# Performance work log

Measured on AMD Instinct MI355X. Metric: run time of the kernel, lower is better.

The kernel has to match this reference:

```python
import jax, jax.numpy as jnp
import numpy as np

IN, OUT, HID = 1024, 1024, 2048
L = IN + OUT + HID
EPS = 1e-12  # F.normalize default eps


def _make_strength_matrix():
    fwd_s, bwd_s, lat_s, self_s = 1.0, 0.5, 0.3, 0.0
    i = np.arange(L)
    # torch: triu (incl diag) = forward, then tril (incl diag) = backward -> diag ends up backward here
    A = np.where(i[:, None] >= i[None, :], bwd_s, fwd_s).astype(np.float32)
    # lateral blocks (within input, within output, within hidden)
    A[0:IN, 0:IN] = lat_s
    A[IN:IN + OUT, IN:IN + OUT] = lat_s
    A[IN + OUT:L, IN + OUT:L] = lat_s
    A[i, i] = self_s
    return A


def setup_inputs() -> dict:
    key = jax.random.key(0)
    kx, ky, kw = jax.random.split(key, 3)
    B = 1024
    x = jax.random.normal(kx, (B, IN), dtype=jnp.float32)
    y = jax.random.normal(ky, (B, OUT), dtype=jnp.float32)
    W = jax.random.normal(kw, (L, L), dtype=jnp.float32) * 0.01
    idx = jnp.arange(L)
    W = W.at[idx, idx].set(0.0)  # fill_diagonal_(0) at init
    A = jnp.asarray(_make_strength_matrix())
    return {"x": x, "y": y, "W": W, "A": A, "n": 32}


def reference(x, y, W, A, n):
    # clamp_x=True, clamp_y=False, norm_hidden=True, average_window<=0
    B = x.shape[0]
    act0 = jnp.concatenate(
        [x, jnp.zeros_like(y), jnp.zeros((B, HID), dtype=x.dtype)], axis=1
    )  # [B, L]
    mw = W * A.T  # modified weights, loop-invariant

    def step(act, _):
        act = jax.nn.relu(act @ mw.T)          # linear(act, mw) + relu
        act = act.at[:, :IN].set(x)            # clamp_x
        hid = act[:, IN + OUT:]
        nrm = jnp.linalg.norm(hid, axis=1, keepdims=True)
        hid = hid / jnp.maximum(nrm, EPS)      # F.normalize p=2 dim=1
        act = act.at[:, IN + OUT:].set(hid)
        return act, None

    act, _ = jax.lax.scan(step, act0, None, length=n)
    return act
```

## Files before the change

### kernel.cpp

```cpp
#include <hip/hip_runtime.h>
#include <stdint.h>
#include <stddef.h>


#define L 4096
#define INX 1024
#define OUTX 1024
#define BATCH 1024
#define NCOL 3072
#define NITER 32

#define BM 128
#define BN 96
#define BK 64
#define SMEM_BYTES 114688

typedef float floatx4 __attribute__((ext_vector_type(4)));
typedef short bf16x8 __attribute__((ext_vector_type(8)));

__device__ __forceinline__ unsigned short f2bf(float f) {
  unsigned int u = __float_as_uint(f);
  u += 0x7FFF + ((u >> 16) & 1);
  return (unsigned short)(u >> 16);
}
__device__ __forceinline__ float bf2f(unsigned short h) {
  return __uint_as_float(((unsigned int)h) << 16);
}

__device__ __forceinline__ void load_lds_16B(const void* g, void* s) {
  __builtin_amdgcn_global_load_lds(
      (const __attribute__((address_space(1))) unsigned int*)g,
      (__attribute__((address_space(3))) unsigned int*)s, 16, 0, 0);
}

__global__ void prep_mwn(const float* __restrict__ W, unsigned short* __restrict__ mwn) {
  int idx = blockIdx.x * 256 + threadIdx.x;
  int i = idx >> 10;
  int j4 = (idx & 1023) << 2;
  const float4 w = *(const float4*)&W[(size_t)(INX + i) * L + j4];
  const int c = INX + i;
  const int rc = (c < 2048) ? 1 : 2;
  float wv[4] = {w.x, w.y, w.z, w.w};
  unsigned short o[4];
#pragma unroll
  for (int k = 0; k < 4; ++k) {
    int j = j4 + k;
    int rj = (j < 1024) ? 0 : ((j < 2048) ? 1 : 2);
    float a = (j == c) ? 0.0f : ((rj == rc) ? 0.3f : ((j >= c) ? 0.5f : 1.0f));
    o[k] = f2bf(wv[k] * a);
  }
  *(ushort4*)&mwn[(size_t)i * L + j4] = make_ushort4(o[0], o[1], o[2], o[3]);
}

__global__ void init_act(const float* __restrict__ x, unsigned short* __restrict__ actA) {
  int i = blockIdx.x * 256 + threadIdx.x;
  int col = i & (L - 1), row = i >> 12;
  actA[i] = (col < INX) ? f2bf(x[(size_t)row * INX + col]) : (unsigned short)0;
}

__device__ __forceinline__ void stage(unsigned short* As, unsigned short* Bs,
                                      const unsigned short* gA, const unsigned short* gB,
                                      int kb, int t) {
  const int srow = t >> 3, schunk = t & 7;
  const int o = srow * BK + schunk * 8;
  load_lds_16B(gA + kb, &As[o]);
  load_lds_16B(gA + (size_t)32 * L + kb, &As[o + 32 * BK]);
  load_lds_16B(gA + (size_t)64 * L + kb, &As[o + 64 * BK]);
  load_lds_16B(gA + (size_t)96 * L + kb, &As[o + 96 * BK]);
  load_lds_16B(gB + kb, &Bs[o]);
  load_lds_16B(gB + (size_t)32 * L + kb, &Bs[o + 32 * BK]);
  load_lds_16B(gB + (size_t)64 * L + kb, &Bs[o + 64 * BK]);
}

struct FragSet {
  bf16x8 a[2][4];
  bf16x8 b[2][3];
};

__device__ __forceinline__ void frag_read(FragSet& f, const unsigned short* As,
                                          const unsigned short* Bs,
                                          int wm, int wn, int l15, int quad) {
#pragma unroll
  for (int kk = 0; kk < 2; ++kk) {
    const int c = kk * 4 + quad;
#pragma unroll
    for (int mt = 0; mt < 4; ++mt) {
      int r = wm + mt * 16 + l15;
      f.a[kk][mt] = *(const bf16x8*)&As[r * BK + ((c ^ (r & 7)) * 8)];
    }
#pragma unroll
    for (int nt = 0; nt < 3; ++nt) {
      int r = wn + nt * 16 + l15;
      f.b[kk][nt] = *(const bf16x8*)&Bs[r * BK + ((c ^ (r & 7)) * 8)];
    }
  }
}

__device__ __forceinline__ void mfma_from(const FragSet& f, floatx4 acc[4][3]) {
#pragma unroll
  for (int kk = 0; kk < 2; ++kk)
#pragma unroll
    for (int mt = 0; mt < 4; ++mt)
#pragma unroll
      for (int nt = 0; nt < 3; ++nt)
        acc[mt][nt] = __builtin_amdgcn_mfma_f32_16x16x32_bf16(f.a[kk][mt], f.b[kk][nt],
                                                              acc[mt][nt], 0, 0, 0);
}

#define PSTEP(s, ACC)                                                             \
  do {                                                                            \
    if ((s) + 2 < NS) asm volatile("s_waitcnt vmcnt(7)" ::: "memory");            \
    else              asm volatile("s_waitcnt vmcnt(0)" ::: "memory");            \
    asm volatile("s_barrier" ::: "memory");                                       \
    if ((s) + 1 < NS)                                                             \
      frag_read(fs[((s) + 1) & 1], AsP[((s) + 1) & 3], BsP[((s) + 1) & 3],        \
                wm, wn, l15, quad);                                               \
    if ((s) + 3 < NS)                                                             \
      stage(AsP[((s) + 3) & 3], BsP[((s) + 3) & 3], gA, gB,                       \
            KB0 + ((s) + 3) * BK, t);                                             \
    mfma_from(fs[(s) & 1], ACC);                                                  \
  } while (0)

template<int MODE>
__global__ __launch_bounds__(256, 1) void gemm_k(
    const unsigned short* __restrict__ act,
    const unsigned short* __restrict__ mwn,
    unsigned short* __restrict__ actn,
    unsigned short* __restrict__ c0,
    const float* __restrict__ nsq_prev,
    float* __restrict__ nsq_next) {
  extern __shared__ unsigned short smem[];
  unsigned short* const AsP[4] = {smem, smem + 8192, smem + 16384, smem + 24576};
  unsigned short* const BsP[4] = {smem + 32768, smem + 38912, smem + 45056,
                                  smem + 51200};

  const int t = threadIdx.x;
  const int lane = t & 63;
  const int wave = t >> 6;
  const int wm = (wave >> 1) * 64;
  const int wn = (wave & 1) * 48;
  const int l15 = lane & 15;
  const int quad = lane >> 4;

  const int b = blockIdx.y * 32 + blockIdx.x;
  const int n_idx = (b & 7) * 4 + ((b >> 3) & 3);
  const int m_idx = b >> 5;
  const int m0 = m_idx * BM;
  const int n0 = n_idx * BN;

  const int srow = t >> 3;
  const int schunk = t & 7;
  const int gchunk = schunk ^ (srow & 7);
  const unsigned short* gA = act + (size_t)(m0 + srow) * L + gchunk * 8;
  const unsigned short* gB = mwn + (size_t)(n0 + srow) * L + gchunk * 8;

  const int KB0 = MODE ? INX : 0;
  constexpr int NS = MODE ? 48 : 16;

  floatx4 accA[4][3], accB[4][3];
#pragma unroll
  for (int i = 0; i < 4; ++i)
#pragma unroll
    for (int j = 0; j < 3; ++j) {
      accA[i][j] = (floatx4){0.f, 0.f, 0.f, 0.f};
      if (MODE) accB[i][j] = (floatx4){0.f, 0.f, 0.f, 0.f};
    }

  FragSet fs[2];

  stage(AsP[0], BsP[0], gA, gB, KB0, t);
  stage(AsP[1], BsP[1], gA, gB, KB0 + BK, t);
  stage(AsP[2], BsP[2], gA, gB, KB0 + 2 * BK, t);
  asm volatile("s_waitcnt vmcnt(14)" ::: "memory");
  asm volatile("s_barrier" ::: "memory");
  frag_read(fs[0], AsP[0], BsP[0], wm, wn, l15, quad);

  PSTEP(0, accA);  PSTEP(1, accA);  PSTEP(2, accA);  PSTEP(3, accA);
  PSTEP(4, accA);  PSTEP(5, accA);  PSTEP(6, accA);  PSTEP(7, accA);
  PSTEP(8, accA);  PSTEP(9, accA);  PSTEP(10, accA); PSTEP(11, accA);
  PSTEP(12, accA); PSTEP(13, accA); PSTEP(14, accA); PSTEP(15, accA);
  if (MODE) {
    PSTEP(16, accB); PSTEP(17, accB); PSTEP(18, accB); PSTEP(19, accB);
    PSTEP(20, accB); PSTEP(21, accB); PSTEP(22, accB); PSTEP(23, accB);
    PSTEP(24, accB); PSTEP(25, accB); PSTEP(26, accB); PSTEP(27, accB);
    PSTEP(28, accB); PSTEP(29, accB); PSTEP(30, accB); PSTEP(31, accB);
    PSTEP(32, accB); PSTEP(33, accB); PSTEP(34, accB); PSTEP(35, accB);
    PSTEP(36, accB); PSTEP(37, accB); PSTEP(38, accB); PSTEP(39, accB);
    PSTEP(40, accB); PSTEP(41, accB); PSTEP(42, accB); PSTEP(43, accB);
    PSTEP(44, accB); PSTEP(45, accB); PSTEP(46, accB); PSTEP(47, accB);
  }

  if (MODE == 0) {
    alignas(16) unsigned short buf[48];
#pragma unroll
    for (int mt = 0; mt < 4; ++mt)
#pragma unroll
      for (int nt = 0; nt < 3; ++nt)
#pragma unroll
        for (int r = 0; r < 4; ++r)
          buf[mt * 12 + nt * 4 + r] = f2bf(accA[mt][nt][r]);
    unsigned short* p = c0 + ((size_t)b * 256 + t) * 48;
#pragma unroll
    for (int k = 0; k < 6; ++k)
      *(bf16x8*)&p[k * 8] = *(const bf16x8*)&buf[k * 8];
    return;
  }

  alignas(16) unsigned short c0s[48];
  {
    const unsigned short* p = c0 + ((size_t)b * 256 + t) * 48;
#pragma unroll
    for (int k = 0; k < 6; ++k)
      *(bf16x8*)&c0s[k * 8] = *(const bf16x8*)&p[k * 8];
  }

  float sm[4][4];
#pragma unroll
  for (int mt = 0; mt < 4; ++mt)
#pragma unroll
    for (int r = 0; r < 4; ++r) {
      const int gm = m0 + wm + mt * 16 + quad * 4 + r;
      sm[mt][r] = 1.0f / fmaxf(sqrtf(nsq_prev[gm]), 1e-12f);
    }

  const bool has_hid = (n0 + wn + 48) > OUTX;
#pragma unroll
  for (int mt = 0; mt < 4; ++mt) {
    float ss[4] = {0.f, 0.f, 0.f, 0.f};
#pragma unroll
    for (int nt = 0; nt < 3; ++nt) {
      const int gn = n0 + wn + nt * 16 + l15;
      const bool hid = gn >= OUTX;
#pragma unroll
      for (int r = 0; r < 4; ++r) {
        const int gm = m0 + wm + mt * 16 + quad * 4 + r;
        float v = bf2f(c0s[mt * 12 + nt * 4 + r]) + accA[mt][nt][r]
                  + sm[mt][r] * accB[mt][nt][r];
        v = fmaxf(v, 0.f);
        actn[(size_t)gm * L + INX + gn] = f2bf(v);
        if (hid) ss[r] += v * v;
      }
    }
    if (has_hid) {
#pragma unroll
      for (int r = 0; r < 4; ++r) {
        float sv = ss[r];
        sv += __shfl_xor(sv, 1);
        sv += __shfl_xor(sv, 2);
        sv += __shfl_xor(sv, 4);
        sv += __shfl_xor(sv, 8);
        if (l15 == 0)
          atomicAdd(&nsq_next[m0 + wm + mt * 16 + quad * 4 + r], sv);
      }
    }
  }
}

__global__ void finalize(const float* __restrict__ x, const unsigned short* __restrict__ act,
                         const float* __restrict__ nsq_fin, float* __restrict__ out) {
  int i = blockIdx.x * 256 + threadIdx.x;
  int col = i & (L - 1), row = i >> 12;
  float v;
  if (col < INX) {
    v = x[(size_t)row * INX + col];
  } else {
    v = bf2f(act[i]);
    if (col >= INX + OUTX) v *= 1.0f / fmaxf(sqrtf(nsq_fin[row]), 1e-12f);
  }
  out[i] = v;
}

extern "C" void kernel_launch(void* const* d_in, const int* in_sizes, int n_in,
                              void* d_out, int out_size, void* d_ws, size_t ws_size,
                              hipStream_t stream) {
  const float* x = (const float*)d_in[0];
  const float* W = (const float*)d_in[2];
  float* out = (float*)d_out;

  char* ws = (char*)d_ws;
  unsigned short* mwn  = (unsigned short*)(ws);
  unsigned short* actA = (unsigned short*)(ws + 25165824);
  unsigned short* actB = (unsigned short*)(ws + 33554432);
  unsigned short* c0   = (unsigned short*)(ws + 41943040);
  float* normsq        = (float*)(ws + 48234496);

  static bool attr_done = false;
  if (!attr_done) {
    (void)hipFuncSetAttribute(reinterpret_cast<const void*>(&gemm_k<0>),
                              hipFuncAttributeMaxDynamicSharedMemorySize, SMEM_BYTES);
    (void)hipFuncSetAttribute(reinterpret_cast<const void*>(&gemm_k<1>),
                              hipFuncAttributeMaxDynamicSharedMemorySize, SMEM_BYTES);
    attr_done = true;
  }

  hipMemsetAsync(normsq, 0, (NITER + 1) * BATCH * sizeof(float), stream);
  prep_mwn<<<(NCOL * (L / 4)) / 256, 256, 0, stream>>>(W, mwn);
  init_act<<<(BATCH * L) / 256, 256, 0, stream>>>(x, actA);

  gemm_k<0><<<dim3(32, 8), 256, SMEM_BYTES, stream>>>(actA, mwn, nullptr, c0,
                                                      nullptr, nullptr);

  unsigned short* cur = actA;
  unsigned short* nxt = actB;
  for (int it = 0; it < NITER; ++it) {
    gemm_k<1><<<dim3(32, 8), 256, SMEM_BYTES, stream>>>(
        cur, mwn, nxt, c0, normsq + it * BATCH, normsq + (it + 1) * BATCH);
    unsigned short* tmp = cur; cur = nxt; nxt = tmp;
  }
  finalize<<<(BATCH * L) / 256, 256, 0, stream>>>(x, cur, normsq + NITER * BATCH, out);
}
```

Measured before the change: 1.109 ms.

## Halve GEMM M-tile to 64 rows with 2-wave blocks and triple-buffered static LDS

Shrinks the block tile from 128x96 to 64x96, using 128-thread blocks of two waves each covering 48 columns, and launches twice as many blocks (512 instead of 256) with two blocks per CU. The LDS pipeline drops from four dynamic buffers to three static buffers, with a rotating buffer index in the step macro and an added lgkmcnt wait before each barrier. The aim is better CU fill and occupancy on a 256-CU device, where 256 blocks at one per CU left little latency hiding. In exchange, each block reloads more of the weight tile per output element, and the extra wait may serialize LDS reads.

```diff
diff --git a/kernel.cpp b/kernel.cpp
--- a/kernel.cpp
+++ b/kernel.cpp
@@ -10,10 +10,9 @@
 #define NCOL 3072
 #define NITER 32
 
-#define BM 128
+#define BM 64
 #define BN 96
 #define BK 64
-#define SMEM_BYTES 114688
 
 typedef float floatx4 __attribute__((ext_vector_type(4)));
 typedef short bf16x8 __attribute__((ext_vector_type(8)));
@@ -64,12 +63,15 @@
   const int srow = t >> 3, schunk = t & 7;
   const int o = srow * BK + schunk * 8;
   load_lds_16B(gA + kb, &As[o]);
+  load_lds_16B(gA + (size_t)16 * L + kb, &As[o + 16 * BK]);
   load_lds_16B(gA + (size_t)32 * L + kb, &As[o + 32 * BK]);
-  load_lds_16B(gA + (size_t)64 * L + kb, &As[o + 64 * BK]);
-  load_lds_16B(gA + (size_t)96 * L + kb, &As[o + 96 * BK]);
+  load_lds_16B(gA + (size_t)48 * L + kb, &As[o + 48 * BK]);
   load_lds_16B(gB + kb, &Bs[o]);
+  load_lds_16B(gB + (size_t)16 * L + kb, &Bs[o + 16 * BK]);
   load_lds_16B(gB + (size_t)32 * L + kb, &Bs[o + 32 * BK]);
+  load_lds_16B(gB + (size_t)48 * L + kb, &Bs[o + 48 * BK]);
   load_lds_16B(gB + (size_t)64 * L + kb, &Bs[o + 64 * BK]);
+  load_lds_16B(gB + (size_t)80 * L + kb, &Bs[o + 80 * BK]);
 }
 
 struct FragSet {
@@ -79,13 +81,13 @@
 
 __device__ __forceinline__ void frag_read(FragSet& f, const unsigned short* As,
                                           const unsigned short* Bs,
-                                          int wm, int wn, int l15, int quad) {
+                                          int wn, int l15, int quad) {
 #pragma unroll
   for (int kk = 0; kk < 2; ++kk) {
     const int c = kk * 4 + quad;
 #pragma unroll
     for (int mt = 0; mt < 4; ++mt) {
-      int r = wm + mt * 16 + l15;
+      int r = mt * 16 + l15;
       f.a[kk][mt] = *(const bf16x8*)&As[r * BK + ((c ^ (r & 7)) * 8)];
     }
 #pragma unroll
@@ -107,44 +109,40 @@
                                                               acc[mt][nt], 0, 0, 0);
 }
 
-#define PSTEP(s, ACC)                                                             \
+#define PSTEP(s, SB, FB, ACC)                                                     \
   do {                                                                            \
-    if ((s) + 2 < NS) asm volatile("s_waitcnt vmcnt(7)" ::: "memory");            \
+    if ((s) + 2 < NS) asm volatile("s_waitcnt vmcnt(10)" ::: "memory");           \
     else              asm volatile("s_waitcnt vmcnt(0)" ::: "memory");            \
+    asm volatile("s_waitcnt lgkmcnt(0)" ::: "memory");                            \
     asm volatile("s_barrier" ::: "memory");                                       \
     if ((s) + 1 < NS)                                                             \
-      frag_read(fs[((s) + 1) & 1], AsP[((s) + 1) & 3], BsP[((s) + 1) & 3],        \
-                wm, wn, l15, quad);                                               \
+      frag_read(fs[((s) + 1) & 1], As##FB, Bs##FB, wn, l15, quad);                \
     if ((s) + 3 < NS)                                                             \
-      stage(AsP[((s) + 3) & 3], BsP[((s) + 3) & 3], gA, gB,                       \
-            KB0 + ((s) + 3) * BK, t);                                             \
+      stage(As##SB, Bs##SB, gA, gB, KB0 + ((s) + 3) * BK, t);                     \
     mfma_from(fs[(s) & 1], ACC);                                                  \
   } while (0)
 
 template<int MODE>
-__global__ __launch_bounds__(256, 1) void gemm_k(
+__global__ __launch_bounds__(128, 2) void gemm_k(
     const unsigned short* __restrict__ act,
     const unsigned short* __restrict__ mwn,
     unsigned short* __restrict__ actn,
     unsigned short* __restrict__ c0,
     const float* __restrict__ nsq_prev,
     float* __restrict__ nsq_next) {
-  extern __shared__ unsigned short smem[];
-  unsigned short* const AsP[4] = {smem, smem + 8192, smem + 16384, smem + 24576};
-  unsigned short* const BsP[4] = {smem + 32768, smem + 38912, smem + 45056,
-                                  smem + 51200};
+  __shared__ alignas(16) unsigned short As0[BM * BK], As1[BM * BK], As2[BM * BK];
+  __shared__ alignas(16) unsigned short Bs0[BN * BK], Bs1[BN * BK], Bs2[BN * BK];
 
   const int t = threadIdx.x;
   const int lane = t & 63;
   const int wave = t >> 6;
-  const int wm = (wave >> 1) * 64;
-  const int wn = (wave & 1) * 48;
+  const int wn = wave * 48;
   const int l15 = lane & 15;
   const int quad = lane >> 4;
 
   const int b = blockIdx.y * 32 + blockIdx.x;
-  const int n_idx = (b & 7) * 4 + ((b >> 3) & 3);
-  const int m_idx = b >> 5;
+  const int n_idx = (b & 7) * 4 + (b >> 7);
+  const int m_idx = (b >> 3) & 15;
   const int m0 = m_idx * BM;
   const int n0 = n_idx * BN;
 
@@ -168,26 +166,31 @@
 
   FragSet fs[2];
 
-  stage(AsP[0], BsP[0], gA, gB, KB0, t);
-  stage(AsP[1], BsP[1], gA, gB, KB0 + BK, t);
-  stage(AsP[2], BsP[2], gA, gB, KB0 + 2 * BK, t);
-  asm volatile("s_waitcnt vmcnt(14)" ::: "memory");
+  stage(As0, Bs0, gA, gB, KB0, t);
+  stage(As1, Bs1, gA, gB, KB0 + BK, t);
+  stage(As2, Bs2, gA, gB, KB0 + 2 * BK, t);
+  asm volatile("s_waitcnt vmcnt(20)" ::: "memory");
   asm volatile("s_barrier" ::: "memory");
-  frag_read(fs[0], AsP[0], BsP[0], wm, wn, l15, quad);
-
-  PSTEP(0, accA);  PSTEP(1, accA);  PSTEP(2, accA);  PSTEP(3, accA);
-  PSTEP(4, accA);  PSTEP(5, accA);  PSTEP(6, accA);  PSTEP(7, accA);
-  PSTEP(8, accA);  PSTEP(9, accA);  PSTEP(10, accA); PSTEP(11, accA);
-  PSTEP(12, accA); PSTEP(13, accA); PSTEP(14, accA); PSTEP(15, accA);
+  frag_read(fs[0], As0, Bs0, wn, l15, quad);
+
+  PSTEP(0, 0, 1, accA);  PSTEP(1, 1, 2, accA);  PSTEP(2, 2, 0, accA);
+  PSTEP(3, 0, 1, accA);  PSTEP(4, 1, 2, accA);  PSTEP(5, 2, 0, accA);
+  PSTEP(6, 0, 1, accA);  PSTEP(7, 1, 2, accA);  PSTEP(8, 2, 0, accA);
+  PSTEP(9, 0, 1, accA);  PSTEP(10, 1, 2, accA); PSTEP(11, 2, 0, accA);
+  PSTEP(12, 0, 1, accA); PSTEP(13, 1, 2, accA); PSTEP(14, 2, 0, accA);
+  PSTEP(15, 0, 1, accA);
   if (MODE) {
-    PSTEP(16, accB); PSTEP(17, accB); PSTEP(18, accB); PSTEP(19, accB);
-    PSTEP(20, accB); PSTEP(21, accB); PSTEP(22, accB); PSTEP(23, accB);
-    PSTEP(24, accB); PSTEP(25, accB); PSTEP(26, accB); PSTEP(27, accB);
-    PSTEP(28, accB); PSTEP(29, accB); PSTEP(30, accB); PSTEP(31, accB);
-    PSTEP(32, accB); PSTEP(33, accB); PSTEP(34, accB); PSTEP(35, accB);
-    PSTEP(36, accB); PSTEP(37, accB); PSTEP(38, accB); PSTEP(39, accB);
-    PSTEP(40, accB); PSTEP(41, accB); PSTEP(42, accB); PSTEP(43, accB);
-    PSTEP(44, accB); PSTEP(45, accB); PSTEP(46, accB); PSTEP(47, accB);
+    PSTEP(16, 1, 2, accB); PSTEP(17, 2, 0, accB); PSTEP(18, 0, 1, accB);
+    PSTEP(19, 1, 2, accB); PSTEP(20, 2, 0, accB); PSTEP(21, 0, 1, accB);
+    PSTEP(22, 1, 2, accB); PSTEP(23, 2, 0, accB); PSTEP(24, 0, 1, accB);
+    PSTEP(25, 1, 2, accB); PSTEP(26, 2, 0, accB); PSTEP(27, 0, 1, accB);
+    PSTEP(28, 1, 2, accB); PSTEP(29, 2, 0, accB); PSTEP(30, 0, 1, accB);
+    PSTEP(31, 1, 2, accB); PSTEP(32, 2, 0, accB); PSTEP(33, 0, 1, accB);
+    PSTEP(34, 1, 2, accB); PSTEP(35, 2, 0, accB); PSTEP(36, 0, 1, accB);
+    PSTEP(37, 1, 2, accB); PSTEP(38, 2, 0, accB); PSTEP(39, 0, 1, accB);
+    PSTEP(40, 1, 2, accB); PSTEP(41, 2, 0, accB); PSTEP(42, 0, 1, accB);
+    PSTEP(43, 1, 2, accB); PSTEP(44, 2, 0, accB); PSTEP(45, 0, 1, accB);
+    PSTEP(46, 1, 2, accB); PSTEP(47, 2, 0, accB);
   }
 
   if (MODE == 0) {
@@ -199,7 +202,7 @@
 #pragma unroll
         for (int r = 0; r < 4; ++r)
           buf[mt * 12 + nt * 4 + r] = f2bf(accA[mt][nt][r]);
-    unsigned short* p = c0 + ((size_t)b * 256 + t) * 48;
+    unsigned short* p = c0 + ((size_t)b * 128 + t) * 48;
 #pragma unroll
     for (int k = 0; k < 6; ++k)
       *(bf16x8*)&p[k * 8] = *(const bf16x8*)&buf[k * 8];
@@ -208,7 +211,7 @@
 
   alignas(16) unsigned short c0s[48];
   {
-    const unsigned short* p = c0 + ((size_t)b * 256 + t) * 48;
+    const unsigned short* p = c0 + ((size_t)b * 128 + t) * 48;
 #pragma unroll
     for (int k = 0; k < 6; ++k)
       *(bf16x8*)&c0s[k * 8] = *(const bf16x8*)&p[k * 8];
@@ -219,7 +222,7 @@
   for (int mt = 0; mt < 4; ++mt)
 #pragma unroll
     for (int r = 0; r < 4; ++r) {
-      const int gm = m0 + wm + mt * 16 + quad * 4 + r;
+      const int gm = m0 + mt * 16 + quad * 4 + r;
       sm[mt][r] = 1.0f / fmaxf(sqrtf(nsq_prev[gm]), 1e-12f);
     }
 
@@ -233,7 +236,7 @@
       const bool hid = gn >= OUTX;
 #pragma unroll
       for (int r = 0; r < 4; ++r) {
-        const int gm = m0 + wm + mt * 16 + quad * 4 + r;
+        const int gm = m0 + mt * 16 + quad * 4 + r;
         float v = bf2f(c0s[mt * 12 + nt * 4 + r]) + accA[mt][nt][r]
                   + sm[mt][r] * accB[mt][nt][r];
         v = fmaxf(v, 0.f);
@@ -250,7 +253,7 @@
         sv += __shfl_xor(sv, 4);
         sv += __shfl_xor(sv, 8);
         if (l15 == 0)
-          atomicAdd(&nsq_next[m0 + wm + mt * 16 + quad * 4 + r], sv);
+          atomicAdd(&nsq_next[m0 + mt * 16 + quad * 4 + r], sv);
       }
     }
   }
@@ -284,26 +287,17 @@
   unsigned short* c0   = (unsigned short*)(ws + 41943040);
   float* normsq        = (float*)(ws + 48234496);
 
-  static bool attr_done = false;
-  if (!attr_done) {
-    (void)hipFuncSetAttribute(reinterpret_cast<const void*>(&gemm_k<0>),
-                              hipFuncAttributeMaxDynamicSharedMemorySize, SMEM_BYTES);
-    (void)hipFuncSetAttribute(reinterpret_cast<const void*>(&gemm_k<1>),
-                              hipFuncAttributeMaxDynamicSharedMemorySize, SMEM_BYTES);
-    attr_done = true;
-  }
-
   hipMemsetAsync(normsq, 0, (NITER + 1) * BATCH * sizeof(float), stream);
   prep_mwn<<<(NCOL * (L / 4)) / 256, 256, 0, stream>>>(W, mwn);
   init_act<<<(BATCH * L) / 256, 256, 0, stream>>>(x, actA);
 
-  gemm_k<0><<<dim3(32, 8), 256, SMEM_BYTES, stream>>>(actA, mwn, nullptr, c0,
-                                                      nullptr, nullptr);
+  gemm_k<0><<<dim3(32, 16), 128, 0, stream>>>(actA, mwn, nullptr, c0,
+                                              nullptr, nullptr);
 
   unsigned short* cur = actA;
   unsigned short* nxt = actB;
   for (int it = 0; it < NITER; ++it) {
-    gemm_k<1><<<dim3(32, 8), 256, SMEM_BYTES, stream>>>(
+    gemm_k<1><<<dim3(32, 16), 128, 0, stream>>>(
         cur, mwn, nxt, c0, normsq + it * BATCH, normsq + (it + 1) * BATCH);
     unsigned short* tmp = cur; cur = nxt; nxt = tmp;
   }
```

New measurement: 1.209 ms. 9.1% more time.
